# Kernel optimization log

Hardware: AMD Instinct MI355X
Metric: run time of the kernel (lower is better)

Reference implementation:

```python
import jax, jax.numpy as jnp
import numpy as np

B, S, E, H = 4, 8192, 1024, 16
D = E // H  # head_dim = 64


def setup_inputs() -> dict:
    key = jax.random.key(0)
    ks = jax.random.split(key, 9)
    s = 0.02
    return {
        "x": jax.random.normal(ks[0], (B, S, E), dtype=jnp.float32),
        "Wq": jax.random.normal(ks[1], (D, E), dtype=jnp.float32) * s,
        "bq": jax.random.normal(ks[2], (D,), dtype=jnp.float32) * s,
        "Wk": jax.random.normal(ks[3], (D, E), dtype=jnp.float32) * s,
        "bk": jax.random.normal(ks[4], (D,), dtype=jnp.float32) * s,
        "Wv": jax.random.normal(ks[5], (D, E), dtype=jnp.float32) * s,
        "bv": jax.random.normal(ks[6], (D,), dtype=jnp.float32) * s,
        "Wo": jax.random.normal(ks[7], (E, E), dtype=jnp.float32) * s,
        "bo": jax.random.normal(ks[8], (E,), dtype=jnp.float32) * s,
    }


def reference(x, Wq, bq, Wk, bk, Wv, bv, Wo, bo):
    b, s, e = x.shape
    d = Wq.shape[0]          # head_dim (projections map embed_dim -> head_dim)
    h = e // d               # num_heads
    # torch Linear: y = x @ W.T + b ; projected shape [B, S, d]
    # view(B, -1, h, d) on [B, S, d] => effective seq S' = S // h (faithful to source)
    def split_heads(t):
        return t.reshape(b, -1, h, d).transpose(0, 2, 1, 3)  # [B, H, S', D]
    q = split_heads(x @ Wq.T + bq)
    k = split_heads(x @ Wk.T + bk)
    v = split_heads(x @ Wv.T + bv)
    scores = jnp.einsum('bhqd,bhkd->bhqk', q, k) / np.sqrt(d).astype(jnp.float32)
    attn = jax.nn.softmax(scores, axis=-1)  # dropout=0.0 => identity
    ctx = jnp.einsum('bhqk,bhkd->bhqd', attn, v)
    ctx = ctx.transpose(0, 2, 1, 3).reshape(b, -1, e)  # [B, S', E]
    return ctx @ Wo.T + bo
```

## Files before the change

### kernel.cpp

```cpp
#include <hip/hip_runtime.h>


typedef unsigned short u16;
typedef __attribute__((ext_vector_type(8))) short short8;
typedef __attribute__((ext_vector_type(4))) float f32x4;

__device__ inline u16 f2bf(float f) {
    union { float f; unsigned u; } v; v.f = f;
    unsigned u = v.u;
    return (u16)((u + 0x7fffu + ((u >> 16) & 1u)) >> 16);
}

__global__ __launch_bounds__(256) void convw(
    const float* __restrict__ Wq, const float* __restrict__ bq,
    const float* __restrict__ Wk, const float* __restrict__ bk,
    const float* __restrict__ Wv, const float* __restrict__ bv,
    const float* __restrict__ Wo,
    u16* __restrict__ Wqkv, float* __restrict__ qkvb, u16* __restrict__ Wob)
{
    const int idx = blockIdx.x * 256 + threadIdx.x;
    Wob[idx] = f2bf(Wo[idx]);
    if (idx < 196608) {
        const int row = idx >> 10, k = idx & 1023;
        float v = (row < 64)  ? Wq[row * 1024 + k] * 0.125f
                : (row < 128) ? Wk[(row - 64) * 1024 + k]
                              : Wv[(row - 128) * 1024 + k];
        Wqkv[idx] = f2bf(v);
    }
    if (idx < 192) {
        qkvb[idx] = (idx < 64) ? bq[idx] * 0.125f
                  : (idx < 128) ? bk[idx - 64] : bv[idx - 128];
    }
}

__global__ __launch_bounds__(256) void qkv_gemm(
    const float* __restrict__ X, const u16* __restrict__ W,
    const float* __restrict__ bias, u16* __restrict__ Out)
{
    __shared__ short8 As[4 * 64];
    __shared__ short8 Bs[12 * 64];

    const int tid = threadIdx.x;
    const int lane = tid & 63, wid = tid >> 6;
    const long m0 = (long)blockIdx.x * 64;

    const int ra = tid >> 2;
    const int ka = tid & 3;
    const int aslot = (ra >> 4) * 64 + ka * 16 + (ra & 15);
    const float* px = X + (m0 + ra) * 1024 + ka * 8;

    f32x4 acc[12] = {};

    for (int k0 = 0; k0 < 1024; k0 += 32) {
        float4 x0 = *(const float4*)(px + k0);
        float4 x1 = *(const float4*)(px + k0 + 4);
        short8 av;
        av[0] = (short)f2bf(x0.x); av[1] = (short)f2bf(x0.y);
        av[2] = (short)f2bf(x0.z); av[3] = (short)f2bf(x0.w);
        av[4] = (short)f2bf(x1.x); av[5] = (short)f2bf(x1.y);
        av[6] = (short)f2bf(x1.z); av[7] = (short)f2bf(x1.w);
        short8 bv[3];
        #pragma unroll
        for (int i = 0; i < 3; ++i) {
            const int c = tid + 256 * i;
            bv[i] = *(const short8*)(W + (long)(c >> 2) * 1024 + k0 + (c & 3) * 8);
        }
        __syncthreads();
        As[aslot] = av;
        #pragma unroll
        for (int i = 0; i < 3; ++i) {
            const int c = tid + 256 * i, rb = c >> 2;
            Bs[(rb >> 4) * 64 + (c & 3) * 16 + (rb & 15)] = bv[i];
        }
        __syncthreads();
        short8 af = As[wid * 64 + lane];
        #pragma unroll
        for (int nt = 0; nt < 12; ++nt)
            acc[nt] = __builtin_amdgcn_mfma_f32_16x16x32_bf16(
                af, Bs[nt * 64 + lane], acc[nt], 0, 0, 0);
    }

    const int q = lane >> 4, r = lane & 15;
    #pragma unroll
    for (int nt = 0; nt < 12; ++nt) {
        const int col = nt * 16 + r;
        const float badd = bias[col];
        #pragma unroll
        for (int e = 0; e < 4; ++e) {
            const long row = m0 + wid * 16 + q * 4 + e;
            Out[row * 192 + col] = f2bf(acc[nt][e] + badd);
        }
    }
}

template <typename TC>
__global__ __launch_bounds__(256) void gemm_bf(
    const u16* __restrict__ A, long lda, long sAzH, long sAzL,
    const u16* __restrict__ B, long ldb, long sBzH, long sBzL,
    const float* __restrict__ bias,
    TC* __restrict__ C, long ldc, long sCzH, long sCzL,
    int K)
{
    __shared__ short8 As[4 * 64];
    __shared__ short8 Bs[4 * 64];

    const int tid = threadIdx.x;
    const int lane = tid & 63, wid = tid >> 6;
    const long m0 = (long)blockIdx.x * 64, n0 = (long)blockIdx.y * 64;
    const int zH = blockIdx.z >> 4, zL = blockIdx.z & 15;
    A += zH * sAzH + zL * sAzL;
    B += zH * sBzH + zL * sBzL;
    C += zH * sCzH + zL * sCzL;

    const int r4 = tid >> 2, k8 = tid & 3;
    const int slot = (r4 >> 4) * 64 + k8 * 16 + (r4 & 15);
    const u16* pa = A + (m0 + r4) * lda + k8 * 8;
    const u16* pb = B + (n0 + r4) * ldb + k8 * 8;

    const int mh = (wid >> 1) * 2;
    const int nh = (wid & 1) * 2;

    f32x4 acc[2][2] = {};

    for (int k0 = 0; k0 < K; k0 += 32) {
        short8 av = *(const short8*)(pa + k0);
        short8 bv = *(const short8*)(pb + k0);
        __syncthreads();
        As[slot] = av; Bs[slot] = bv;
        __syncthreads();
        short8 af0 = As[(mh + 0) * 64 + lane], af1 = As[(mh + 1) * 64 + lane];
        short8 bf0 = Bs[(nh + 0) * 64 + lane], bf1 = Bs[(nh + 1) * 64 + lane];
        acc[0][0] = __builtin_amdgcn_mfma_f32_16x16x32_bf16(af0, bf0, acc[0][0], 0, 0, 0);
        acc[0][1] = __builtin_amdgcn_mfma_f32_16x16x32_bf16(af0, bf1, acc[0][1], 0, 0, 0);
        acc[1][0] = __builtin_amdgcn_mfma_f32_16x16x32_bf16(af1, bf0, acc[1][0], 0, 0, 0);
        acc[1][1] = __builtin_amdgcn_mfma_f32_16x16x32_bf16(af1, bf1, acc[1][1], 0, 0, 0);
    }

    const int q = lane >> 4, r = lane & 15;
    #pragma unroll
    for (int i = 0; i < 2; ++i) {
        #pragma unroll
        for (int j = 0; j < 2; ++j) {
            const long col = n0 + (nh + j) * 16 + r;
            const float badd = bias ? bias[col] : 0.0f;
            #pragma unroll
            for (int e = 0; e < 4; ++e) {
                const long row = m0 + (mh + i) * 16 + q * 4 + e;
                float v = acc[i][j][e] + badd;
                if constexpr (sizeof(TC) == 2) C[row * ldc + col] = (TC)f2bf(v);
                else                           C[row * ldc + col] = v;
            }
        }
    }
}

__global__ __launch_bounds__(256) void vtrans(
    const u16* __restrict__ qkv, u16* __restrict__ Vt)
{
    __shared__ u16 T[64][68];
    const int bh = blockIdx.x, b = bh >> 4, h = bh & 15;
    const int i0 = blockIdx.y * 64;
    const int tid = threadIdx.x;

    #pragma unroll
    for (int it = 0; it < 2; ++it) {
        const int c = tid + 256 * it;
        const int il = c >> 3, d8 = (c & 7) * 8;
        short8 v = *(const short8*)(qkv +
            ((long)b * 8192 + (long)(i0 + il) * 16 + h) * 192 + 128 + d8);
        #pragma unroll
        for (int j = 0; j < 8; ++j) T[d8 + j][il] = (u16)v[j];
    }
    __syncthreads();
    #pragma unroll
    for (int it = 0; it < 2; ++it) {
        const int c = tid + 256 * it;
        const int dl = c >> 3, i8 = (c & 7) * 8;
        short8 o;
        #pragma unroll
        for (int j = 0; j < 8; ++j) o[j] = (short)T[dl][i8 + j];
        *(short8*)(Vt + ((long)bh * 64 + dl) * 512 + i0 + i8) = o;
    }
}

__global__ __launch_bounds__(256) void softmax_bf(
    const float* __restrict__ S, u16* __restrict__ P)
{
    const long row = (long)blockIdx.x * 4 + (threadIdx.x >> 6);
    const int lane = threadIdx.x & 63;
    const float* p = S + row * 512;

    float e[8], m = -1e30f;
    #pragma unroll
    for (int j = 0; j < 8; ++j) { e[j] = p[lane + 64 * j]; m = fmaxf(m, e[j]); }
    #pragma unroll
    for (int off = 32; off; off >>= 1) m = fmaxf(m, __shfl_xor(m, off, 64));
    float s = 0.f;
    #pragma unroll
    for (int j = 0; j < 8; ++j) { e[j] = __expf(e[j] - m); s += e[j]; }
    #pragma unroll
    for (int off = 32; off; off >>= 1) s += __shfl_xor(s, off, 64);
    const float inv = 1.0f / s;
    u16* o = P + row * 512;
    #pragma unroll
    for (int j = 0; j < 8; ++j) o[lane + 64 * j] = f2bf(e[j] * inv);
}

extern "C" void kernel_launch(void* const* d_in, const int* in_sizes, int n_in,
                              void* d_out, int out_size, void* d_ws, size_t ws_size,
                              hipStream_t stream)
{
    const float* x  = (const float*)d_in[0];
    const float* Wq = (const float*)d_in[1];
    const float* bq = (const float*)d_in[2];
    const float* Wk = (const float*)d_in[3];
    const float* bk = (const float*)d_in[4];
    const float* Wv = (const float*)d_in[5];
    const float* bv = (const float*)d_in[6];
    const float* Wo = (const float*)d_in[7];
    const float* bo = (const float*)d_in[8];
    float* out = (float*)d_out;
    char* ws = (char*)d_ws;

    u16*   qkv  = (u16*)(ws);
    u16*   Vt   = (u16*)(ws + 12582912);
    u16*   Wqkv = (u16*)(ws + 16777216);
    u16*   Wob  = (u16*)(ws + 17170432);
    float* qkvb = (float*)(ws + 19267584);
    u16*   ctx  = (u16*)(ws + 19268352);
    float* sc   = (float*)(ws + 23462656);

    const size_t need_batched = 23462656ull + 67108864ull + 33554432ull;
    const bool batched = ws_size >= need_batched;

    convw<<<4096, 256, 0, stream>>>(Wq, bq, Wk, bk, Wv, bv, Wo, Wqkv, qkvb, Wob);
    qkv_gemm<<<512, 256, 0, stream>>>(x, Wqkv, qkvb, qkv);
    vtrans<<<dim3(64, 8), 256, 0, stream>>>(qkv, Vt);

    if (batched) {
        u16* P = (u16*)(ws + 23462656 + 67108864);
        gemm_bf<float><<<dim3(8, 8, 64), 256, 0, stream>>>(
            qkv,      3072, 8192L * 192, 192,
            qkv + 64, 3072, 8192L * 192, 192,
            nullptr,
            sc, 512, 16L * 262144, 262144, 64);
        softmax_bf<<<8192, 256, 0, stream>>>(sc, P);
        gemm_bf<u16><<<dim3(8, 1, 64), 256, 0, stream>>>(
            P,  512, 16L * 262144, 262144,
            Vt, 512, 16L * 32768,  32768,
            nullptr,
            ctx, 1024, 524288, 64, 512);
    } else {
        u16* P = (u16*)(ws + 23462656 + 16777216);
        for (int b = 0; b < 4; ++b) {
            const u16* qb = qkv + (long)b * 8192 * 192;
            gemm_bf<float><<<dim3(8, 8, 16), 256, 0, stream>>>(
                qb,      3072, 0, 192,
                qb + 64, 3072, 0, 192,
                nullptr,
                sc, 512, 0, 262144, 64);
            softmax_bf<<<2048, 256, 0, stream>>>(sc, P);
            gemm_bf<u16><<<dim3(8, 1, 16), 256, 0, stream>>>(
                P,  512, 0, 262144,
                Vt + (long)b * 524288, 512, 0, 32768,
                nullptr,
                ctx + (long)b * 524288, 1024, 0, 64, 512);
        }
    }

    gemm_bf<float><<<dim3(32, 16, 1), 256, 0, stream>>>(
        ctx, 1024, 0, 0,
        Wob, 1024, 0, 0,
        bo,
        out, 1024, 0, 0, 1024);
}
```

Before: 302.4 us.

## Fuse QK^T, softmax and PV into a single flash-attention kernel

Replaces the three-stage attention path (score GEMM writing fp32 scores, a separate softmax pass, then a PV GEMM) with one flash-style kernel. It computes scores in registers with MFMA, keeps an online softmax with running max and sum, stages P through a small per-wave LDS tile, and accumulates P·V directly. This removes the large fp32 score and bf16 P round trips through global memory and two launches. The new kernel loads K and V straight from global memory with no LDS sharing across waves, and its grid is only 512 blocks. Separately, the x-to-bf16 conversion in the QKV GEMM now uses a packed bf16x2 intrinsic instead of per-element manual rounding.

```diff
diff --git a/kernel.cpp b/kernel.cpp
--- a/kernel.cpp
+++ b/kernel.cpp
@@ -1,4 +1,5 @@
 #include <hip/hip_runtime.h>
+#include <hip/hip_bf16.h>
 
 
 typedef unsigned short u16;
@@ -9,6 +10,11 @@
     union { float f; unsigned u; } v; v.f = f;
     unsigned u = v.u;
     return (u16)((u + 0x7fffu + ((u >> 16) & 1u)) >> 16);
+}
+__device__ inline unsigned pack_bf2(float a, float b) {
+    union { __hip_bfloat162 h; unsigned u; } v;
+    v.h = __float22bfloat162_rn(float2{a, b});
+    return v.u;
 }
 
 __global__ __launch_bounds__(256) void convw(
@@ -54,11 +60,11 @@
     for (int k0 = 0; k0 < 1024; k0 += 32) {
         float4 x0 = *(const float4*)(px + k0);
         float4 x1 = *(const float4*)(px + k0 + 4);
-        short8 av;
-        av[0] = (short)f2bf(x0.x); av[1] = (short)f2bf(x0.y);
-        av[2] = (short)f2bf(x0.z); av[3] = (short)f2bf(x0.w);
-        av[4] = (short)f2bf(x1.x); av[5] = (short)f2bf(x1.y);
-        av[6] = (short)f2bf(x1.z); av[7] = (short)f2bf(x1.w);
+        union { short8 s; unsigned u[4]; } av;
+        av.u[0] = pack_bf2(x0.x, x0.y);
+        av.u[1] = pack_bf2(x0.z, x0.w);
+        av.u[2] = pack_bf2(x1.x, x1.y);
+        av.u[3] = pack_bf2(x1.z, x1.w);
         short8 bv[3];
         #pragma unroll
         for (int i = 0; i < 3; ++i) {
@@ -66,7 +72,7 @@
             bv[i] = *(const short8*)(W + (long)(c >> 2) * 1024 + k0 + (c & 3) * 8);
         }
         __syncthreads();
-        As[aslot] = av;
+        As[aslot] = av.s;
         #pragma unroll
         for (int i = 0; i < 3; ++i) {
             const int c = tid + 256 * i, rb = c >> 2;
@@ -93,13 +99,130 @@
     }
 }
 
-template <typename TC>
+__global__ __launch_bounds__(256) void vtrans(
+    const u16* __restrict__ qkv, u16* __restrict__ Vt)
+{
+    __shared__ u16 T[64][68];
+    const int bh = blockIdx.x, b = bh >> 4, h = bh & 15;
+    const int i0 = blockIdx.y * 64;
+    const int tid = threadIdx.x;
+
+    #pragma unroll
+    for (int it = 0; it < 2; ++it) {
+        const int c = tid + 256 * it;
+        const int il = c >> 3, d8 = (c & 7) * 8;
+        short8 v = *(const short8*)(qkv +
+            ((long)b * 8192 + (long)(i0 + il) * 16 + h) * 192 + 128 + d8);
+        #pragma unroll
+        for (int j = 0; j < 8; ++j) T[d8 + j][il] = (u16)v[j];
+    }
+    __syncthreads();
+    #pragma unroll
+    for (int it = 0; it < 2; ++it) {
+        const int c = tid + 256 * it;
+        const int dl = c >> 3, i8 = (c & 7) * 8;
+        short8 o;
+        #pragma unroll
+        for (int j = 0; j < 8; ++j) o[j] = (short)T[dl][i8 + j];
+        *(short8*)(Vt + ((long)bh * 64 + dl) * 512 + i0 + i8) = o;
+    }
+}
+
+__global__ __launch_bounds__(256) void attn_flash(
+    const u16* __restrict__ qkv, const u16* __restrict__ Vt,
+    u16* __restrict__ ctx)
+{
+    __shared__ u16 Plds[4][16 * 72];
+
+    const int tid = threadIdx.x, lane = tid & 63, wid = tid >> 6;
+    const int q = lane >> 4, r = lane & 15;
+    const int qt = blockIdx.x;
+    const int bh = blockIdx.y;
+    const int b = bh >> 4, h = bh & 15;
+
+    const long qrowbase = (long)b * 8192 + h;
+
+    short8 Qf0, Qf1;
+    {
+        const int i = qt * 64 + wid * 16 + r;
+        const u16* p = qkv + (qrowbase + (long)i * 16) * 192 + q * 8;
+        Qf0 = *(const short8*)(p);
+        Qf1 = *(const short8*)(p + 32);
+    }
+
+    f32x4 O[4] = {};
+    float mrun[4] = {-1e30f, -1e30f, -1e30f, -1e30f};
+    float lrun[4] = {};
+    u16* Pw = &Plds[wid][0];
+
+    for (int j0 = 0; j0 < 512; j0 += 64) {
+        f32x4 S[4];
+        #pragma unroll
+        for (int ct = 0; ct < 4; ++ct) {
+            const int key = j0 + ct * 16 + r;
+            const u16* p = qkv + (qrowbase + (long)key * 16) * 192 + 64 + q * 8;
+            short8 k0 = *(const short8*)(p);
+            short8 k1 = *(const short8*)(p + 32);
+            f32x4 s = {};
+            s = __builtin_amdgcn_mfma_f32_16x16x32_bf16(Qf0, k0, s, 0, 0, 0);
+            s = __builtin_amdgcn_mfma_f32_16x16x32_bf16(Qf1, k1, s, 0, 0, 0);
+            S[ct] = s;
+        }
+        #pragma unroll
+        for (int e = 0; e < 4; ++e) {
+            float mc = fmaxf(fmaxf(S[0][e], S[1][e]), fmaxf(S[2][e], S[3][e]));
+            #pragma unroll
+            for (int off = 1; off < 16; off <<= 1)
+                mc = fmaxf(mc, __shfl_xor(mc, off, 64));
+            const float mnew = fmaxf(mrun[e], mc);
+            const float alpha = __expf(mrun[e] - mnew);
+            mrun[e] = mnew;
+            float se = 0.f;
+            #pragma unroll
+            for (int ct = 0; ct < 4; ++ct) {
+                const float pv = __expf(S[ct][e] - mnew);
+                S[ct][e] = pv; se += pv;
+            }
+            #pragma unroll
+            for (int off = 1; off < 16; off <<= 1)
+                se += __shfl_xor(se, off, 64);
+            lrun[e] = lrun[e] * alpha + se;
+            #pragma unroll
+            for (int nt = 0; nt < 4; ++nt) O[nt][e] *= alpha;
+        }
+        #pragma unroll
+        for (int e = 0; e < 4; ++e)
+            #pragma unroll
+            for (int ct = 0; ct < 4; ++ct)
+                Pw[(q * 4 + e) * 72 + ct * 16 + r] = f2bf(S[ct][e]);
+        short8 Pf0 = *(const short8*)(Pw + r * 72 + q * 8);
+        short8 Pf1 = *(const short8*)(Pw + r * 72 + 32 + q * 8);
+        #pragma unroll
+        for (int nt = 0; nt < 4; ++nt) {
+            const u16* p = Vt + ((long)bh * 64 + nt * 16 + r) * 512 + j0 + q * 8;
+            short8 v0 = *(const short8*)(p);
+            short8 v1 = *(const short8*)(p + 32);
+            O[nt] = __builtin_amdgcn_mfma_f32_16x16x32_bf16(Pf0, v0, O[nt], 0, 0, 0);
+            O[nt] = __builtin_amdgcn_mfma_f32_16x16x32_bf16(Pf1, v1, O[nt], 0, 0, 0);
+        }
+    }
+
+    #pragma unroll
+    for (int e = 0; e < 4; ++e) {
+        const float inv = 1.0f / lrun[e];
+        const long i = qt * 64 + wid * 16 + q * 4 + e;
+        u16* po = ctx + ((long)b * 512 + i) * 1024 + h * 64 + r;
+        #pragma unroll
+        for (int nt = 0; nt < 4; ++nt)
+            po[nt * 16] = f2bf(O[nt][e] * inv);
+    }
+}
+
 __global__ __launch_bounds__(256) void gemm_bf(
-    const u16* __restrict__ A, long lda, long sAzH, long sAzL,
-    const u16* __restrict__ B, long ldb, long sBzH, long sBzL,
+    const u16* __restrict__ A, long lda,
+    const u16* __restrict__ B, long ldb,
     const float* __restrict__ bias,
-    TC* __restrict__ C, long ldc, long sCzH, long sCzL,
-    int K)
+    float* __restrict__ C, long ldc, int K)
 {
     __shared__ short8 As[4 * 64];
     __shared__ short8 Bs[4 * 64];
@@ -107,19 +230,13 @@
     const int tid = threadIdx.x;
     const int lane = tid & 63, wid = tid >> 6;
     const long m0 = (long)blockIdx.x * 64, n0 = (long)blockIdx.y * 64;
-    const int zH = blockIdx.z >> 4, zL = blockIdx.z & 15;
-    A += zH * sAzH + zL * sAzL;
-    B += zH * sBzH + zL * sBzL;
-    C += zH * sCzH + zL * sCzL;
 
     const int r4 = tid >> 2, k8 = tid & 3;
     const int slot = (r4 >> 4) * 64 + k8 * 16 + (r4 & 15);
     const u16* pa = A + (m0 + r4) * lda + k8 * 8;
     const u16* pb = B + (n0 + r4) * ldb + k8 * 8;
 
-    const int mh = (wid >> 1) * 2;
-    const int nh = (wid & 1) * 2;
-
+    const int mh = (wid >> 1) * 2, nh = (wid & 1) * 2;
     f32x4 acc[2][2] = {};
 
     for (int k0 = 0; k0 < K; k0 += 32) {
@@ -138,72 +255,17 @@
 
     const int q = lane >> 4, r = lane & 15;
     #pragma unroll
-    for (int i = 0; i < 2; ++i) {
+    for (int i = 0; i < 2; ++i)
         #pragma unroll
         for (int j = 0; j < 2; ++j) {
             const long col = n0 + (nh + j) * 16 + r;
-            const float badd = bias ? bias[col] : 0.0f;
+            const float badd = bias[col];
             #pragma unroll
             for (int e = 0; e < 4; ++e) {
                 const long row = m0 + (mh + i) * 16 + q * 4 + e;
-                float v = acc[i][j][e] + badd;
-                if constexpr (sizeof(TC) == 2) C[row * ldc + col] = (TC)f2bf(v);
-                else                           C[row * ldc + col] = v;
+                C[row * ldc + col] = acc[i][j][e] + badd;
             }
         }
-    }
-}
-
-__global__ __launch_bounds__(256) void vtrans(
-    const u16* __restrict__ qkv, u16* __restrict__ Vt)
-{
-    __shared__ u16 T[64][68];
-    const int bh = blockIdx.x, b = bh >> 4, h = bh & 15;
-    const int i0 = blockIdx.y * 64;
-    const int tid = threadIdx.x;
-
-    #pragma unroll
-    for (int it = 0; it < 2; ++it) {
-        const int c = tid + 256 * it;
-        const int il = c >> 3, d8 = (c & 7) * 8;
-        short8 v = *(const short8*)(qkv +
-            ((long)b * 8192 + (long)(i0 + il) * 16 + h) * 192 + 128 + d8);
-        #pragma unroll
-        for (int j = 0; j < 8; ++j) T[d8 + j][il] = (u16)v[j];
-    }
-    __syncthreads();
-    #pragma unroll
-    for (int it = 0; it < 2; ++it) {
-        const int c = tid + 256 * it;
-        const int dl = c >> 3, i8 = (c & 7) * 8;
-        short8 o;
-        #pragma unroll
-        for (int j = 0; j < 8; ++j) o[j] = (short)T[dl][i8 + j];
-        *(short8*)(Vt + ((long)bh * 64 + dl) * 512 + i0 + i8) = o;
-    }
-}
-
-__global__ __launch_bounds__(256) void softmax_bf(
-    const float* __restrict__ S, u16* __restrict__ P)
-{
-    const long row = (long)blockIdx.x * 4 + (threadIdx.x >> 6);
-    const int lane = threadIdx.x & 63;
-    const float* p = S + row * 512;
-
-    float e[8], m = -1e30f;
-    #pragma unroll
-    for (int j = 0; j < 8; ++j) { e[j] = p[lane + 64 * j]; m = fmaxf(m, e[j]); }
-    #pragma unroll
-    for (int off = 32; off; off >>= 1) m = fmaxf(m, __shfl_xor(m, off, 64));
-    float s = 0.f;
-    #pragma unroll
-    for (int j = 0; j < 8; ++j) { e[j] = __expf(e[j] - m); s += e[j]; }
-    #pragma unroll
-    for (int off = 32; off; off >>= 1) s += __shfl_xor(s, off, 64);
-    const float inv = 1.0f / s;
-    u16* o = P + row * 512;
-    #pragma unroll
-    for (int j = 0; j < 8; ++j) o[lane + 64 * j] = f2bf(e[j] * inv);
 }
 
 extern "C" void kernel_launch(void* const* d_in, const int* in_sizes, int n_in,
@@ -228,49 +290,11 @@
     u16*   Wob  = (u16*)(ws + 17170432);
     float* qkvb = (float*)(ws + 19267584);
     u16*   ctx  = (u16*)(ws + 19268352);
-    float* sc   = (float*)(ws + 23462656);
-
-    const size_t need_batched = 23462656ull + 67108864ull + 33554432ull;
-    const bool batched = ws_size >= need_batched;
 
     convw<<<4096, 256, 0, stream>>>(Wq, bq, Wk, bk, Wv, bv, Wo, Wqkv, qkvb, Wob);
     qkv_gemm<<<512, 256, 0, stream>>>(x, Wqkv, qkvb, qkv);
     vtrans<<<dim3(64, 8), 256, 0, stream>>>(qkv, Vt);
-
-    if (batched) {
-        u16* P = (u16*)(ws + 23462656 + 67108864);
-        gemm_bf<float><<<dim3(8, 8, 64), 256, 0, stream>>>(
-            qkv,      3072, 8192L * 192, 192,
-            qkv + 64, 3072, 8192L * 192, 192,
-            nullptr,
-            sc, 512, 16L * 262144, 262144, 64);
-        softmax_bf<<<8192, 256, 0, stream>>>(sc, P);
-        gemm_bf<u16><<<dim3(8, 1, 64), 256, 0, stream>>>(
-            P,  512, 16L * 262144, 262144,
-            Vt, 512, 16L * 32768,  32768,
-            nullptr,
-            ctx, 1024, 524288, 64, 512);
-    } else {
-        u16* P = (u16*)(ws + 23462656 + 16777216);
-        for (int b = 0; b < 4; ++b) {
-            const u16* qb = qkv + (long)b * 8192 * 192;
-            gemm_bf<float><<<dim3(8, 8, 16), 256, 0, stream>>>(
-                qb,      3072, 0, 192,
-                qb + 64, 3072, 0, 192,
-                nullptr,
-                sc, 512, 0, 262144, 64);
-            softmax_bf<<<2048, 256, 0, stream>>>(sc, P);
-            gemm_bf<u16><<<dim3(8, 1, 16), 256, 0, stream>>>(
-                P,  512, 0, 262144,
-                Vt + (long)b * 524288, 512, 0, 32768,
-                nullptr,
-                ctx + (long)b * 524288, 1024, 0, 64, 512);
-        }
-    }
-
-    gemm_bf<float><<<dim3(32, 16, 1), 256, 0, stream>>>(
-        ctx, 1024, 0, 0,
-        Wob, 1024, 0, 0,
-        bo,
-        out, 1024, 0, 0, 1024);
-}
+    attn_flash<<<dim3(8, 64), 256, 0, stream>>>(qkv, Vt, ctx);
+    gemm_bf<<<dim3(32, 16), 256, 0, stream>>>(
+        ctx, 1024, Wob, 1024, bo, out, 1024, 1024);
+}
```

Measured after the change: 285.0 us. -5.7%, faster.
